# Optimization experiments

Hardware: AMD Instinct MI355X
Metric: run time of the kernel (lower is better)

Reference implementation:

```python
import jax, jax.numpy as jnp
import numpy as np
import math

B, S, IN_DIM = 8, 1024, 64
OUT_DIM, NB = 128, 6
LN_EPS = 1e-5

def setup_inputs() -> dict:
    key = jax.random.key(0)
    k1, k2, k3, k4 = jax.random.split(key, 4)
    seq = jax.random.normal(k1, (B, S, IN_DIM), dtype=jnp.float32)
    # torch inits: M ~ U(-0.5,0.5), P ~ U(-0.1,0.1), residual_proj.weight ~ U(-0.1,0.1)
    M = jax.random.uniform(k2, (OUT_DIM, IN_DIM), minval=-0.5, maxval=0.5, dtype=jnp.float32)
    P = jax.random.uniform(k3, (OUT_DIM, OUT_DIM, NB), minval=-0.1, maxval=0.1, dtype=jnp.float32)
    res_W = jax.random.uniform(k4, (OUT_DIM, IN_DIM), minval=-0.1, maxval=0.1, dtype=jnp.float32)
    gamma = jnp.ones((OUT_DIM,), dtype=jnp.float32)
    beta = jnp.zeros((OUT_DIM,), dtype=jnp.float32)
    return {"seq": seq, "M": M, "P": P, "res_W": res_W, "gamma": gamma, "beta": beta}

def _layer(x, M, P, res_W, gamma, beta):
    b, s, _ = x.shape
    out_dim, _, nb = P.shape
    # x_trans = x @ M.T then LayerNorm over last dim
    x_t = jnp.einsum('bsj,ij->bsi', x, M)  # (b,s,out)
    mu = jnp.mean(x_t, axis=-1, keepdims=True)
    var = jnp.mean((x_t - mu) ** 2, axis=-1, keepdims=True)
    x_n = (x_t - mu) * jax.lax.rsqrt(var + LN_EPS) * gamma + beta
    # periods[i,j,g] = i*(out*nb) + j*nb + g + 2
    periods = (jnp.arange(out_dim * out_dim * nb, dtype=jnp.float32) + 2.0).reshape(out_dim, out_dim, nb)
    pos = jnp.arange(s, dtype=jnp.float32)
    phi = jnp.cos((2.0 * math.pi) * pos[:, None, None, None] / periods[None])  # (s,out,out,nb)
    # Nk[b,s,i] = sum_{j,g} P[i,j,g] * x_n[b,s,j] * phi[s,i,j,g]
    W = jnp.einsum('ijg,sijg->sij', P, phi)      # (s,out,out) position-dependent mixing
    Nk = jnp.einsum('bsj,sij->bsi', x_n, W)      # (b,s,out)
    residual = jnp.einsum('bsj,ij->bsi', x, res_W)  # 'separate' residual projection
    return Nk + residual

def reference(seq, M, P, res_W, gamma, beta):
    return _layer(seq, M, P, res_W, gamma, beta)
```

## Files before the change

### kernel.cpp

```cpp
#include <hip/hip_runtime.h>
#include <math.h>

#define BD 8
#define SD 1024
#define ID 64
#define OD 128
#define NBD 6
#define TI 4
#define SCH 32
#define SS 8
#define WPAD 136
#define NU (SCH / SS)

typedef short bf16x8 __attribute__((ext_vector_type(8)));
typedef float f32x4 __attribute__((ext_vector_type(4)));
typedef ushort ushortx8 __attribute__((ext_vector_type(8)));

__device__ __forceinline__ ushort rne_bf16(float f) {
    union { float f; unsigned u; } cv; cv.f = f;
    return (ushort)((cv.u + 0x7FFFu + ((cv.u >> 16) & 1u)) >> 16);
}
__device__ __forceinline__ float bf16_to_f(ushort u) {
    union { unsigned u; float f; } cv; cv.u = ((unsigned)u) << 16;
    return cv.f;
}
__device__ __forceinline__ bf16x8 pack8(float4 a, float4 b) {
    union { ushort u[8]; bf16x8 v; } p;
    p.u[0] = rne_bf16(a.x); p.u[1] = rne_bf16(a.y);
    p.u[2] = rne_bf16(a.z); p.u[3] = rne_bf16(a.w);
    p.u[4] = rne_bf16(b.x); p.u[5] = rne_bf16(b.y);
    p.u[6] = rne_bf16(b.z); p.u[7] = rne_bf16(b.w);
    return p.v;
}
__device__ __forceinline__ void pack8_split(float4 a, float4 b,
                                            bf16x8* hi, bf16x8* lo) {
    union { ushort u[8]; bf16x8 v; } ph, pl;
    const float e[8] = {a.x, a.y, a.z, a.w, b.x, b.y, b.z, b.w};
    #pragma unroll
    for (int k = 0; k < 8; ++k) {
        const ushort h = rne_bf16(e[k]);
        ph.u[k] = h;
        pl.u[k] = rne_bf16(e[k] - bf16_to_f(h));
    }
    *hi = ph.v; *lo = pl.v;
}

__global__ __launch_bounds__(256) void ln_mfma(
    const float* __restrict__ seq,
    const float* __restrict__ M,
    const float* __restrict__ resW,
    const float* __restrict__ gamma,
    const float* __restrict__ beta,
    ushort* __restrict__ xnT,
    float* __restrict__ resid)
{
    const int t   = threadIdx.x;
    const int r   = blockIdx.x & 7;
    const int k   = blockIdx.x >> 3;
    const int scl = r * 4 + (k >> 4);
    const int s0  = scl * SCH + (k & 15) * 2;

    const int w  = t >> 6;
    const int l  = t & 63;
    const int lr = l & 15;
    const int lk = l >> 4;

    __shared__ float Ct[16][132];

    bf16x8 ahi[2], alo[2];
    {
        const int ba = lr & 7, sa = lr >> 3;
        const float* __restrict__ arow = &seq[(ba * SD + s0 + sa) * ID];
        #pragma unroll
        for (int ka = 0; ka < 2; ++ka) {
            const float4 v0 = *(const float4*)&arow[ka * 32 + lk * 8];
            const float4 v1 = *(const float4*)&arow[ka * 32 + lk * 8 + 4];
            pack8_split(v0, v1, &ahi[ka], &alo[ka]);
        }
    }
    bf16x8 bfr[2][2][2];
    #pragma unroll
    for (int mat = 0; mat < 2; ++mat) {
        const float* __restrict__ Wm = mat ? resW : M;
        #pragma unroll
        for (int ct = 0; ct < 2; ++ct) {
            const float* __restrict__ wrow = &Wm[(w * 32 + ct * 16 + lr) * ID];
            #pragma unroll
            for (int kb = 0; kb < 2; ++kb) {
                const float4 v0 = *(const float4*)&wrow[kb * 32 + lk * 8];
                const float4 v1 = *(const float4*)&wrow[kb * 32 + lk * 8 + 4];
                bfr[mat][ct][kb] = pack8(v0, v1);
            }
        }
    }

    f32x4 accx[2], accr[2];
    #pragma unroll
    for (int ct = 0; ct < 2; ++ct) {
        f32x4 a4 = {0.f, 0.f, 0.f, 0.f};
        a4 = __builtin_amdgcn_mfma_f32_16x16x32_bf16(alo[0], bfr[0][ct][0], a4, 0, 0, 0);
        a4 = __builtin_amdgcn_mfma_f32_16x16x32_bf16(alo[1], bfr[0][ct][1], a4, 0, 0, 0);
        a4 = __builtin_amdgcn_mfma_f32_16x16x32_bf16(ahi[0], bfr[0][ct][0], a4, 0, 0, 0);
        a4 = __builtin_amdgcn_mfma_f32_16x16x32_bf16(ahi[1], bfr[0][ct][1], a4, 0, 0, 0);
        accx[ct] = a4;
        f32x4 r4 = {0.f, 0.f, 0.f, 0.f};
        r4 = __builtin_amdgcn_mfma_f32_16x16x32_bf16(ahi[0], bfr[1][ct][0], r4, 0, 0, 0);
        r4 = __builtin_amdgcn_mfma_f32_16x16x32_bf16(ahi[1], bfr[1][ct][1], r4, 0, 0, 0);
        accr[ct] = r4;
    }

    #pragma unroll
    for (int ct = 0; ct < 2; ++ct)
        #pragma unroll
        for (int q = 0; q < 4; ++q) {
            const int rr = lk * 4 + q;
            const int b = rr & 7, sl = rr >> 3;
            resid[((s0 + sl) * BD + b) * OD + w * 32 + ct * 16 + lr] = accr[ct][q];
        }
    #pragma unroll
    for (int ct = 0; ct < 2; ++ct)
        #pragma unroll
        for (int q = 0; q < 4; ++q)
            Ct[lk * 4 + q][w * 32 + ct * 16 + lr] = accx[ct][q];
    __syncthreads();

    {
        const int row = t >> 4;
        const int c0  = (t & 15) * 8;
        float sum = 0.f, ssq = 0.f;
        #pragma unroll
        for (int e = 0; e < 8; ++e) {
            const float v = Ct[row][c0 + e];
            sum += v; ssq = fmaf(v, v, ssq);
        }
        #pragma unroll
        for (int m = 1; m < 16; m <<= 1) {
            sum += __shfl_xor(sum, m, 64);
            ssq += __shfl_xor(ssq, m, 64);
        }
        const float mu   = sum * (1.0f / OD);
        const float vr   = ssq * (1.0f / OD) - mu * mu;
        const float rstd = rsqrtf(vr + 1e-5f);

        const float4 g0 = *(const float4*)&gamma[c0];
        const float4 g1 = *(const float4*)&gamma[c0 + 4];
        const float4 b0 = *(const float4*)&beta[c0];
        const float4 b1 = *(const float4*)&beta[c0 + 4];
        const float gv[8] = {g0.x,g0.y,g0.z,g0.w,g1.x,g1.y,g1.z,g1.w};
        const float bv[8] = {b0.x,b0.y,b0.z,b0.w,b1.x,b1.y,b1.z,b1.w};

        union { ushort u[8]; ushortx8 v; } xo;
        #pragma unroll
        for (int e = 0; e < 8; ++e) {
            const float xv = (Ct[row][c0 + e] - mu) * rstd * gv[e] + bv[e];
            xo.u[e] = rne_bf16(xv);
        }
        const int b  = row & 7, sl = row >> 3;
        *(ushortx8*)&xnT[((s0 + sl) * BD + b) * OD + c0] = xo.v;
    }
}

__global__ __launch_bounds__(512, 6) void nk_kernel(
    const float* __restrict__ P,
    const ushort* __restrict__ xnT,
    const float* __restrict__ resid,
    float* __restrict__ out)
{
    const int r  = blockIdx.x & 7;
    const int k  = blockIdx.x >> 3;
    const int sc = r * 4 + (k >> 5);
    const int i0 = (k & 31) * TI;

    const int t  = threadIdx.x;
    const int iw = t >> 7;
    const int jb = t & 127;
    const int wv = t >> 6;
    const int l  = t & 63;

    __shared__ ushort Wl[SS][TI][WPAD];
    __shared__ ushort Xl[SS][BD][WPAD];
    __shared__ float  Cst[SS][BD][TI];

    const int st_ii = t & 3;
    const int st_b  = (t >> 2) & 7;
    const int st_sl = t >> 5;

    float Pv[NBD], kk[NBD], c0[NBD], c1[NBD];
    const int ig = i0 + iw;
    const float s0f = (float)(sc * SCH);
    #pragma unroll
    for (int g = 0; g < NBD; ++g) {
        Pv[g] = P[(ig * OD + jb) * NBD + g];
        const float per = (float)(ig * (OD * NBD) + jb * NBD + g + 2);
        const float rp  = __builtin_amdgcn_rcpf(per);
        kk[g] = 2.0f * __builtin_amdgcn_cosf(rp);
        c1[g] = __builtin_amdgcn_cosf(__builtin_amdgcn_fractf(s0f * rp));
        c0[g] = __builtin_amdgcn_cosf(__builtin_amdgcn_fractf((s0f - 1.0f) * rp));
    }

    for (int u = 0; u < NU; ++u) {
        const int sb = sc * SCH + u * SS;

        float rv = 0.f;
        if (t < SS * BD * TI)
            rv = resid[((sb + st_sl) * BD + st_b) * OD + i0 + st_ii];

        {
            const uint4* __restrict__ src = (const uint4*)(xnT + sb * (BD * OD));
            #pragma unroll
            for (int rr = 0; rr < 2; ++rr) {
                const int e  = t + 512 * rr;
                const uint4 v = src[e];
                const int eo = e << 3;
                const int si = eo >> 10;
                const int b  = (eo >> 7) & 7;
                const int j0 = eo & 127;
                *(uint4*)&Xl[si][b][j0] = v;
            }
        }
        #pragma unroll
        for (int ssi = 0; ssi < SS; ++ssi) {
            float wvv = 0.f;
            #pragma unroll
            for (int g = 0; g < NBD; ++g) wvv = fmaf(Pv[g], c1[g], wvv);
            #pragma unroll
            for (int g = 0; g < NBD; ++g) {
                const float cn = fmaf(kk[g], c1[g], -c0[g]);
                c0[g] = c1[g]; c1[g] = cn;
            }
            Wl[ssi][iw][jb] = rne_bf16(wvv);
        }
        __syncthreads();

        {
            f32x4 acc4 = {0.f, 0.f, 0.f, 0.f};
            #pragma unroll
            for (int m = 0; m < 4; ++m) {
                const bf16x8 a = *(const bf16x8*)&Xl[wv][l & 7][m * 32 + (l >> 4) * 8];
                const bf16x8 b = *(const bf16x8*)&Wl[wv][l & 3][m * 32 + (l >> 4) * 8];
                acc4 = __builtin_amdgcn_mfma_f32_16x16x32_bf16(a, b, acc4, 0, 0, 0);
            }
            const int col  = l & 15;
            const int rowg = l >> 4;
            if (col < TI && rowg < 2) {
                #pragma unroll
                for (int q = 0; q < 4; ++q)
                    Cst[wv][rowg * 4 + q][col] = acc4[q];
            }
        }
        __syncthreads();

        if (t < SS * BD * TI)
            out[(st_b * SD + sb + st_sl) * OD + i0 + st_ii] = Cst[st_sl][st_b][st_ii] + rv;
    }
}

extern "C" void kernel_launch(void* const* d_in, const int* in_sizes, int n_in,
                              void* d_out, int out_size, void* d_ws, size_t ws_size,
                              hipStream_t stream) {
    const float* seq   = (const float*)d_in[0];
    const float* M     = (const float*)d_in[1];
    const float* P     = (const float*)d_in[2];
    const float* resW  = (const float*)d_in[3];
    const float* gamma = (const float*)d_in[4];
    const float* beta  = (const float*)d_in[5];
    float* out = (float*)d_out;

    ushort* xnT   = (ushort*)d_ws;
    float*  resid = (float*)(xnT + SD * BD * OD);

    ln_mfma<<<dim3(SD / 2), dim3(256), 0, stream>>>(seq, M, resW, gamma, beta,
                                                    xnT, resid);
    nk_kernel<<<dim3((SD / SCH) * (OD / TI)), dim3(512), 0, stream>>>(
        P, xnT, resid, out);
}
```

Measured before the change: 24.61 us.

## Load MFMA A-fragments directly from global and prefetch P into cache

The nk kernel no longer stages the normalized activations through shared memory. Each wave now loads its bf16 A-fragments straight from global memory into registers, which removes the LDS write and read and shrinks the shared-memory footprint. Separately, the LayerNorm kernel now touches every element of P with dummy loads so that P is warm in L2/MALL before nk_kernel reads it. The cost is uncoalesced-ish per-lane global loads in the hot loop and extra traffic in the first kernel.

New measurement: 31.66 us. 28.6% more time.

```diff
diff --git a/kernel.cpp b/kernel.cpp
--- a/kernel.cpp
+++ b/kernel.cpp
@@ -49,6 +49,7 @@
     const float* __restrict__ seq,
     const float* __restrict__ M,
     const float* __restrict__ resW,
+    const float* __restrict__ P,
     const float* __restrict__ gamma,
     const float* __restrict__ beta,
     ushort* __restrict__ xnT,
@@ -158,6 +159,15 @@
         const int b  = row & 7, sl = row >> 3;
         *(ushortx8*)&xnT[((s0 + sl) * BD + b) * OD + c0] = xo.v;
     }
+
+    {
+        const int idx = (blockIdx.x >> 3) * 256 + t;
+        #pragma unroll
+        for (int m = 0; m < 6; ++m) {
+            const float v = P[idx + m * 16384];
+            asm volatile("" :: "v"(v));
+        }
+    }
 }
 
 __global__ __launch_bounds__(512, 6) void nk_kernel(
@@ -178,7 +188,6 @@
     const int l  = t & 63;
 
     __shared__ ushort Wl[SS][TI][WPAD];
-    __shared__ ushort Xl[SS][BD][WPAD];
     __shared__ float  Cst[SS][BD][TI];
 
     const int st_ii = t & 3;
@@ -198,26 +207,21 @@
         c0[g] = __builtin_amdgcn_cosf(__builtin_amdgcn_fractf((s0f - 1.0f) * rp));
     }
 
+    const ushort* __restrict__ abase = xnT + (l & 7) * OD + (l >> 4) * 8;
+
     for (int u = 0; u < NU; ++u) {
         const int sb = sc * SCH + u * SS;
+
+        const ushort* __restrict__ arow = abase + (sb + wv) * (BD * OD);
+        const bf16x8 af0 = *(const bf16x8*)&arow[0];
+        const bf16x8 af1 = *(const bf16x8*)&arow[32];
+        const bf16x8 af2 = *(const bf16x8*)&arow[64];
+        const bf16x8 af3 = *(const bf16x8*)&arow[96];
 
         float rv = 0.f;
         if (t < SS * BD * TI)
             rv = resid[((sb + st_sl) * BD + st_b) * OD + i0 + st_ii];
 
-        {
-            const uint4* __restrict__ src = (const uint4*)(xnT + sb * (BD * OD));
-            #pragma unroll
-            for (int rr = 0; rr < 2; ++rr) {
-                const int e  = t + 512 * rr;
-                const uint4 v = src[e];
-                const int eo = e << 3;
-                const int si = eo >> 10;
-                const int b  = (eo >> 7) & 7;
-                const int j0 = eo & 127;
-                *(uint4*)&Xl[si][b][j0] = v;
-            }
-        }
         #pragma unroll
         for (int ssi = 0; ssi < SS; ++ssi) {
             float wvv = 0.f;
@@ -234,12 +238,14 @@
 
         {
             f32x4 acc4 = {0.f, 0.f, 0.f, 0.f};
-            #pragma unroll
-            for (int m = 0; m < 4; ++m) {
-                const bf16x8 a = *(const bf16x8*)&Xl[wv][l & 7][m * 32 + (l >> 4) * 8];
-                const bf16x8 b = *(const bf16x8*)&Wl[wv][l & 3][m * 32 + (l >> 4) * 8];
-                acc4 = __builtin_amdgcn_mfma_f32_16x16x32_bf16(a, b, acc4, 0, 0, 0);
-            }
+            const bf16x8 b0 = *(const bf16x8*)&Wl[wv][l & 3][0  + (l >> 4) * 8];
+            const bf16x8 b1 = *(const bf16x8*)&Wl[wv][l & 3][32 + (l >> 4) * 8];
+            const bf16x8 b2 = *(const bf16x8*)&Wl[wv][l & 3][64 + (l >> 4) * 8];
+            const bf16x8 b3 = *(const bf16x8*)&Wl[wv][l & 3][96 + (l >> 4) * 8];
+            acc4 = __builtin_amdgcn_mfma_f32_16x16x32_bf16(af0, b0, acc4, 0, 0, 0);
+            acc4 = __builtin_amdgcn_mfma_f32_16x16x32_bf16(af1, b1, acc4, 0, 0, 0);
+            acc4 = __builtin_amdgcn_mfma_f32_16x16x32_bf16(af2, b2, acc4, 0, 0, 0);
+            acc4 = __builtin_amdgcn_mfma_f32_16x16x32_bf16(af3, b3, acc4, 0, 0, 0);
             const int col  = l & 15;
             const int rowg = l >> 4;
             if (col < TI && rowg < 2) {
@@ -269,7 +275,7 @@
     ushort* xnT   = (ushort*)d_ws;
     float*  resid = (float*)(xnT + SD * BD * OD);
 
-    ln_mfma<<<dim3(SD / 2), dim3(256), 0, stream>>>(seq, M, resW, gamma, beta,
+    ln_mfma<<<dim3(SD / 2), dim3(256), 0, stream>>>(seq, M, resW, P, gamma, beta,
                                                     xnT, resid);
     nk_kernel<<<dim3((SD / SCH) * (OD / TI)), dim3(512), 0, stream>>>(
         P, xnT, resid, out);
```
